# Kernel tuning notes

Measured on AMD Instinct MI355X. Metric: run time of the kernel, lower is better.

The kernel has to match this reference:

```python
import jax, jax.numpy as jnp
import numpy as np


def ternary_quantize(w):
    # threshold = 0.7 * mean(|w|); maps w to {-1, 0, +1}
    threshold = 0.7 * jnp.sum(jnp.abs(w)) / w.size
    return jnp.sign(jnp.sign(w + threshold) + jnp.sign(w - threshold))


def setup_inputs() -> dict:
    key = jax.random.key(0)
    k1, k2, k3 = jax.random.split(key, 3)
    B, N = 4096, 8192
    x = jax.random.normal(k1, (B, N), dtype=jnp.float32)
    kernel = jax.random.normal(k2, (N,), dtype=jnp.float32)
    bias = jax.random.normal(k3, (N,), dtype=jnp.float32)
    return {"x": x, "kernel": kernel, "bias": bias}


def reference(x, kernel, bias):
    # Original: y = x @ diag(ternary(kernel)) + bias.
    # Matmul by a diagonal matrix is exactly a per-column scale; we compute
    # the identical math as a fused elementwise scale + bias add.
    q = ternary_quantize(kernel)          # [N] in {-1, 0, 1}
    return x * q[None, :] + bias[None, :]  # [B, N]
```

## Files before the change

kernel.cpp:

```cpp
#include <hip/hip_runtime.h>

typedef float f32x4 __attribute__((ext_vector_type(4)));

__device__ __forceinline__ void nt_store(f32x4 v, f32x4* p) {
    __builtin_nontemporal_store(v, p);
}

__device__ __forceinline__ float tern(float w, float t) {
    return (fabsf(w) >= t) ? copysignf(1.f, w) : 0.f;
}

__global__ __launch_bounds__(256) void fused_ternary_scale_bias(
    const f32x4* __restrict__ x, const float* __restrict__ w,
    const f32x4* __restrict__ bias4, f32x4* __restrict__ out,
    int n, long total4) {
    __shared__ float red[256];
    const int tid = threadIdx.x;

    float s = 0.f;
    for (int i = tid; i < n; i += 256) s += fabsf(w[i]);
    red[tid] = s;
    __syncthreads();
    for (int off = 128; off > 0; off >>= 1) {
        if (tid < off) red[tid] += red[tid + off];
        __syncthreads();
    }
    const float t = 0.7f * red[0] / (float)n;

    const int n4 = n >> 2;
    const long i0 = (long)blockIdx.x * blockDim.x + tid;
    const long stride = (long)gridDim.x * blockDim.x;
    const int c = (int)(i0 & (long)(n4 - 1));

    const f32x4 wv = reinterpret_cast<const f32x4*>(w)[c];
    f32x4 qv;
    qv.x = tern(wv.x, t);
    qv.y = tern(wv.y, t);
    qv.z = tern(wv.z, t);
    qv.w = tern(wv.w, t);
    const f32x4 bv = bias4[c];

    for (long i = i0; i < total4; i += stride) {
        f32x4 xv = x[i];
        f32x4 o = xv * qv + bv;
        nt_store(o, &out[i]);
    }
}

extern "C" void kernel_launch(void* const* d_in, const int* in_sizes, int n_in,
                              void* d_out, int out_size, void* d_ws, size_t ws_size,
                              hipStream_t stream) {
    const float* x      = (const float*)d_in[0];
    const float* kernel = (const float*)d_in[1];
    const float* bias   = (const float*)d_in[2];
    float* out = (float*)d_out;

    const int N = in_sizes[1];
    const long total4 = (long)out_size / 4;

    fused_ternary_scale_bias<<<2048, 256, 0, stream>>>(
        (const f32x4*)x, kernel, (const f32x4*)bias, (f32x4*)out, N, total4);
}
```

Before: 54.96 us.

## Split threshold reduction into a single-block pre-kernel instead of per-block recompute

The mean-abs reduction over the weight vector was previously recomputed redundantly by all 2048 blocks before streaming. It now runs once in a separate one-block kernel using vectorized loads and wave shuffles, writing the threshold to workspace. The streaming kernel just reads that scalar. This removes redundant reads and syncs per block but adds a second launch and a serial dependency between kernels.

Result: faster. 51.57 us (-6.2%).

```diff
diff --git a/kernel.cpp b/kernel.cpp
--- a/kernel.cpp
+++ b/kernel.cpp
@@ -10,22 +10,35 @@
     return (fabsf(w) >= t) ? copysignf(1.f, w) : 0.f;
 }
 
-__global__ __launch_bounds__(256) void fused_ternary_scale_bias(
+__global__ __launch_bounds__(1024) void threshold_kernel(
+    const float* __restrict__ w, float* __restrict__ t_out, int n) {
+    const int tid = threadIdx.x;
+    const f32x4* w4 = reinterpret_cast<const f32x4*>(w);
+    const int n4 = n >> 2;
+    float s = 0.f;
+    for (int i = tid; i < n4; i += 1024) {
+        const f32x4 v = w4[i];
+        s += fabsf(v.x) + fabsf(v.y) + fabsf(v.z) + fabsf(v.w);
+    }
+    #pragma unroll
+    for (int off = 32; off > 0; off >>= 1) s += __shfl_xor(s, off, 64);
+    __shared__ float partial[16];
+    if ((tid & 63) == 0) partial[tid >> 6] = s;
+    __syncthreads();
+    if (tid == 0) {
+        float tot = 0.f;
+        #pragma unroll
+        for (int k = 0; k < 16; ++k) tot += partial[k];
+        t_out[0] = 0.7f * tot / (float)n;
+    }
+}
+
+__global__ __launch_bounds__(256) void scale_bias_stream(
     const f32x4* __restrict__ x, const float* __restrict__ w,
     const f32x4* __restrict__ bias4, f32x4* __restrict__ out,
-    int n, long total4) {
-    __shared__ float red[256];
+    const float* __restrict__ t_ptr, int n, long total4) {
     const int tid = threadIdx.x;
-
-    float s = 0.f;
-    for (int i = tid; i < n; i += 256) s += fabsf(w[i]);
-    red[tid] = s;
-    __syncthreads();
-    for (int off = 128; off > 0; off >>= 1) {
-        if (tid < off) red[tid] += red[tid + off];
-        __syncthreads();
-    }
-    const float t = 0.7f * red[0] / (float)n;
+    const float t = t_ptr[0];
 
     const int n4 = n >> 2;
     const long i0 = (long)blockIdx.x * blockDim.x + tid;
@@ -54,10 +67,13 @@
     const float* kernel = (const float*)d_in[1];
     const float* bias   = (const float*)d_in[2];
     float* out = (float*)d_out;
+    float* t_ws = (float*)d_ws;
 
     const int N = in_sizes[1];
     const long total4 = (long)out_size / 4;
 
-    fused_ternary_scale_bias<<<2048, 256, 0, stream>>>(
-        (const f32x4*)x, kernel, (const f32x4*)bias, (f32x4*)out, N, total4);
+    threshold_kernel<<<1, 1024, 0, stream>>>(kernel, t_ws, N);
+    scale_bias_stream<<<2048, 256, 0, stream>>>(
+        (const f32x4*)x, kernel, (const f32x4*)bias, (f32x4*)out,
+        t_ws, N, total4);
 }
```
